# Kernel tuning notes

Hardware: AMD Instinct MI355X
Metric: run time of the kernel (lower is better)

Reference implementation:

```python
import jax, jax.numpy as jnp
import numpy as np

HIDDEN = 1024
NUM_HEADS = 16
BATCH = 2
SEQ = 2048


def setup_inputs() -> dict:
    key = jax.random.key(0)
    ks = jax.random.split(key, 5)
    scale = 1.0 / np.sqrt(HIDDEN)
    return {
        "x": jax.random.normal(ks[0], (BATCH, SEQ, HIDDEN), dtype=jnp.float32),
        "W_qkv": jax.random.normal(ks[1], (HIDDEN, 3 * HIDDEN), dtype=jnp.float32) * scale,
        "b_qkv": jax.random.normal(ks[2], (3 * HIDDEN,), dtype=jnp.float32) * 0.02,
        "W_o": jax.random.normal(ks[3], (HIDDEN, HIDDEN), dtype=jnp.float32) * scale,
        "b_o": jax.random.normal(ks[4], (HIDDEN,), dtype=jnp.float32) * 0.02,
    }


def reference(x, W_qkv, b_qkv, W_o, b_o):
    # x: [B, S, H]
    B, S, H = x.shape
    nh = NUM_HEADS
    hs = H // nh
    qkv = jnp.einsum('bsh,hk->bsk', x, W_qkv) + b_qkv  # [B, S, 3H]
    Q, K, V = qkv[..., :H], qkv[..., H:2 * H], qkv[..., 2 * H:]
    # split heads: [B, nh, S, hs]
    Q = Q.reshape(B, S, nh, hs).transpose(0, 2, 1, 3)
    K = K.reshape(B, S, nh, hs).transpose(0, 2, 1, 3)
    V = V.reshape(B, S, nh, hs).transpose(0, 2, 1, 3)
    scores = jnp.einsum('bnqd,bnkd->bnqk', Q, K) / jnp.sqrt(jnp.asarray(hs, x.dtype))
    # NOTE: the original module applies no causal mask despite its name.
    probs = jax.nn.softmax(scores, axis=-1)
    av = jnp.einsum('bnqk,bnkd->bqnd', probs, V)  # [B, S, nh, hs]
    av = av.reshape(B, S, H)
    return jnp.einsum('bsh,ho->bso', av, W_o) + b_o
```

## Files before the change

### kernel.cpp

```cpp
#include <hip/hip_runtime.h>
#include <hip/hip_bf16.h>
#include <stdint.h>

#define HIDDEN 1024
#define NHEAD  16
#define HS     64
#define BATCH  2
#define SEQ    2048
#define MTOT   (BATCH*SEQ)
#define NQKV   (3*HIDDEN)

typedef __hip_bfloat16 bf16;
typedef __attribute__((ext_vector_type(8))) short s16x8;
typedef __attribute__((ext_vector_type(4))) float f32x4;
typedef __attribute__((ext_vector_type(16))) float f32x16;

__device__ __forceinline__ short f2bf(float f) {
  bf16 h = __float2bfloat16(f);
  return *reinterpret_cast<short*>(&h);
}

__device__ __forceinline__ unsigned cvt_pk_bf16(float lo, float hi) {
  unsigned r;
  asm("v_cvt_pk_bf16_f32 %0, %1, %2" : "=v"(r) : "v"(lo), "v"(hi));
  return r;
}

__device__ __forceinline__ int swz(int row, int blk) {
  return (row*8 + (blk ^ (row & 7)))*8;
}

#define GLOAD_LDS(gp, lp) \
  __builtin_amdgcn_global_load_lds((const __attribute__((address_space(1))) void*)(gp), \
                                   (__attribute__((address_space(3))) void*)(lp), 16, 0, 0)

__device__ __forceinline__ int xcd_swz(int orig, int nwg) {
  return (orig & 7)*(nwg >> 3) + (orig >> 3);
}

__global__ void k_cvt_x(const float* __restrict__ x, short* __restrict__ xb, int n8) {
  int i = blockIdx.x*256 + threadIdx.x;
  if (i >= n8) return;
  const f32x4* xv = (const f32x4*)x;
  f32x4 a = xv[2*i], b = xv[2*i+1];
  s16x8 o = { f2bf(a[0]), f2bf(a[1]), f2bf(a[2]), f2bf(a[3]),
              f2bf(b[0]), f2bf(b[1]), f2bf(b[2]), f2bf(b[3]) };
  *(s16x8*)&xb[i*8] = o;
}

__global__ void k_cvt_wT(const float* __restrict__ W, bf16* __restrict__ WT, int K, int N) {
  __shared__ __align__(16) float tile[64][65];
  int n0 = blockIdx.x*64, k0 = blockIdx.y*64;
  int t = threadIdx.x;
  #pragma unroll
  for (int c = 0; c < 4; c++) {
    int s = c*256 + t;
    int r = s >> 4;
    int cc = s & 15;
    f32x4 v = *(const f32x4*)&W[(size_t)(k0 + r)*N + n0 + cc*4];
    tile[r][cc*4+0] = v[0]; tile[r][cc*4+1] = v[1];
    tile[r][cc*4+2] = v[2]; tile[r][cc*4+3] = v[3];
  }
  __syncthreads();
  #pragma unroll
  for (int c = 0; c < 2; c++) {
    int s = c*256 + t;
    int r = s >> 3;
    int cc = s & 7;
    s16x8 o;
    #pragma unroll
    for (int u = 0; u < 8; u++) o[u] = f2bf(tile[cc*8+u][r]);
    *(s16x8*)&WT[(size_t)(n0 + r)*K + k0 + cc*8] = o;
  }
}

template<int OUT_BF16>
__global__ __launch_bounds__(256) void k_gemm(
    const bf16* __restrict__ A, const bf16* __restrict__ BT,
    const float* __restrict__ bias, void* __restrict__ Cout,
    int M, int N, int K)
{
  __shared__ __align__(16) short Asl[128*64];
  __shared__ __align__(16) short Bsl[128*64];
  int t = threadIdx.x;
  int lane = t & 63, w = t >> 6;
  int q = lane & 15, g = lane >> 4;
  int nwg = gridDim.x*gridDim.y;
  int swzid = xcd_swz(blockIdx.y*gridDim.x + blockIdx.x, nwg);
  int bx = swzid % gridDim.x, by = swzid / gridDim.x;
  int row0 = by*128, col0 = bx*128;
  int wr = (w >> 1)*64, wc = (w & 1)*64;

  f32x4 acc[4][4] = {};

  for (int kt = 0; kt < K; kt += 64) {
    __syncthreads();
    #pragma unroll
    for (int c = 0; c < 4; c++) {
      int s = c*256 + t, r = s >> 3, bd = s & 7, bs = bd ^ (r & 7);
      GLOAD_LDS(&A[(size_t)(row0 + r)*K + kt + bs*8], &Asl[s*8]);
      GLOAD_LDS(&BT[(size_t)(col0 + r)*K + kt + bs*8], &Bsl[s*8]);
    }
    __syncthreads();
    #pragma unroll
    for (int kk = 0; kk < 2; kk++) {
      s16x8 af[4], bfr[4];
      #pragma unroll
      for (int i = 0; i < 4; i++) {
        af[i]  = *(const s16x8*)&Asl[swz(wr + i*16 + q, kk*4 + g)];
        bfr[i] = *(const s16x8*)&Bsl[swz(wc + i*16 + q, kk*4 + g)];
      }
      __builtin_amdgcn_s_setprio(1);
      #pragma unroll
      for (int i = 0; i < 4; i++)
        #pragma unroll
        for (int j = 0; j < 4; j++)
          acc[i][j] = __builtin_amdgcn_mfma_f32_16x16x32_bf16(af[i], bfr[j], acc[i][j], 0, 0, 0);
      __builtin_amdgcn_s_setprio(0);
    }
  }
  #pragma unroll
  for (int i = 0; i < 4; i++) {
    #pragma unroll
    for (int j = 0; j < 4; j++) {
      int col = col0 + wc + j*16 + q;
      float bv = bias[col];
      int rowb = row0 + wr + i*16 + g*4;
      #pragma unroll
      for (int r = 0; r < 4; r++) {
        float v = acc[i][j][r] + bv;
        if (OUT_BF16)
          ((bf16*)Cout)[(size_t)(rowb + r)*N + col] = __float2bfloat16(v);
        else
          ((float*)Cout)[(size_t)(rowb + r)*N + col] = v;
      }
    }
  }
}

__global__ void k_repack_v(const bf16* __restrict__ qkv, bf16* __restrict__ Vt) {
  int s0 = blockIdx.x*64;
  int bh = blockIdx.y;
  int b = bh >> 4, h = bh & 15;
  __shared__ __align__(16) short vt[64][68];
  int t = threadIdx.x;
  #pragma unroll
  for (int c = 0; c < 2; c++) {
    int s = c*256 + t, r = s >> 3, bd = s & 7;
    s16x8 v = *(const s16x8*)&qkv[(size_t)(b*SEQ + s0 + r)*NQKV + 2*HIDDEN + h*HS + bd*8];
    #pragma unroll
    for (int u = 0; u < 8; u++) vt[r][bd*8+u] = v[u];
  }
  __syncthreads();
  #pragma unroll
  for (int c = 0; c < 2; c++) {
    int s = c*256 + t, d = s >> 3, bs8 = s & 7;
    s16x8 o;
    #pragma unroll
    for (int u = 0; u < 8; u++) {
      int p = bs8*8 + u;
      int key = (p & ~12) | ((p & 4) << 1) | ((p & 8) >> 1);
      o[u] = vt[key][d];
    }
    *(s16x8*)&Vt[((size_t)(bh*HS + d))*SEQ + s0 + bs8*8] = o;
  }
}

struct AttnState {
  float psum;
  f32x16 oacc0, oacc1;
};

__device__ __forceinline__ void attn_stage(
    const bf16* __restrict__ kbase, const bf16* __restrict__ vbase,
    int kv, int t, short* Ks, short* Vs)
{
  #pragma unroll
  for (int c = 0; c < 4; c++) {
    int s = c*256 + t, r = s >> 3, bd = s & 7, bs = bd ^ (r & 7);
    GLOAD_LDS(&kbase[(size_t)(kv + r)*NQKV + bs*8], &Ks[s*8]);
  }
  #pragma unroll
  for (int c = 0; c < 4; c++) {
    int s = c*256 + t, d = s >> 4, bd = s & 15, bs = bd ^ (d & 15);
    GLOAD_LDS(&vbase[(size_t)d*SEQ + kv + bs*8], &Vs[s*8]);
  }
}

__device__ __forceinline__ void attn_compute(
    const short* Ks, const short* Vs, const s16x8* qf,
    int ql, int hi, AttnState& st)
{
  const float SC2 = 0.125f*1.44269504f;
  const float CB  = -12.f*1.44269504f;
  #pragma unroll
  for (int kb = 0; kb < 4; kb++) {
    f32x16 sf = {};
    __builtin_amdgcn_s_setprio(1);
    #pragma unroll
    for (int ks = 0; ks < 4; ks++) {
      int row = kb*32 + ql;
      int ch = (ks*2 + hi) ^ (row & 7);
      s16x8 a = *(const s16x8*)&Ks[(row*8 + ch)*8];
      sf = __builtin_amdgcn_mfma_f32_32x32x16_bf16(a, qf[ks], sf, 0, 0, 0);
    }
    __builtin_amdgcn_s_setprio(0);

    unsigned pkw[8];
    #pragma unroll
    for (int i = 0; i < 8; i++) {
      float p0 = __builtin_amdgcn_exp2f(__builtin_fmaf(sf[2*i],   SC2, CB));
      float p1 = __builtin_amdgcn_exp2f(__builtin_fmaf(sf[2*i+1], SC2, CB));
      st.psum += p0 + p1;
      pkw[i] = cvt_pk_bf16(p0, p1);
    }

    __builtin_amdgcn_s_setprio(1);
    #pragma unroll
    for (int kq = 0; kq < 2; kq++) {
      union { unsigned u[4]; s16x8 v; } pu;
      pu.u[0] = pkw[kq*4]; pu.u[1] = pkw[kq*4+1];
      pu.u[2] = pkw[kq*4+2]; pu.u[3] = pkw[kq*4+3];
      s16x8 pa = pu.v;
      {
        int row = ql, ch = (kb*4 + kq*2 + hi) ^ (row & 15);
        s16x8 vb = *(const s16x8*)&Vs[(row*16 + ch)*8];
        st.oacc0 = __builtin_amdgcn_mfma_f32_32x32x16_bf16(pa, vb, st.oacc0, 0, 0, 0);
      }
      {
        int row = 32 + ql, ch = (kb*4 + kq*2 + hi) ^ (row & 15);
        s16x8 vb = *(const s16x8*)&Vs[(row*16 + ch)*8];
        st.oacc1 = __builtin_amdgcn_mfma_f32_32x32x16_bf16(pa, vb, st.oacc1, 0, 0, 0);
      }
    }
    __builtin_amdgcn_s_setprio(0);
  }
}

__global__ __launch_bounds__(256) void k_attn(
    const bf16* __restrict__ qkv, const bf16* __restrict__ Vt, bf16* __restrict__ av)
{
  __shared__ __align__(16) short Ks0[128*64], Ks1[128*64];
  __shared__ __align__(16) short Vs0[64*128], Vs1[64*128];
  int t = threadIdx.x;
  int lane = t & 63, w = t >> 6;
  int ql = lane & 31, hi = lane >> 5;
  int nwg = gridDim.x*gridDim.y;
  int swzid = xcd_swz(blockIdx.y*gridDim.x + blockIdx.x, nwg);
  int qt = swzid & 15, bh = swzid >> 4;
  int b = bh >> 4, h = bh & 15;

  const bf16* qrow = qkv + (size_t)(b*SEQ + qt*128 + w*32 + ql)*NQKV + h*HS;
  s16x8 qf[4];
  #pragma unroll
  for (int ks = 0; ks < 4; ks++)
    qf[ks] = *(const s16x8*)&qrow[ks*16 + hi*8];

  AttnState st;
  st.psum = 0.f;
  st.oacc0 = (f32x16){}; st.oacc1 = (f32x16){};

  const bf16* kbase = qkv + (size_t)(b*SEQ)*NQKV + HIDDEN + h*HS;
  const bf16* vbase = Vt + (size_t)(bh*HS)*SEQ;

  attn_stage(kbase, vbase, 0, t, Ks0, Vs0);
  __syncthreads();

  #pragma unroll 1
  for (int tt = 0; tt < SEQ/128; tt += 2) {
    int kv = tt*128;
    if (kv + 128 < SEQ) attn_stage(kbase, vbase, kv + 128, t, Ks1, Vs1);
    attn_compute(Ks0, Vs0, qf, ql, hi, st);
    __syncthreads();
    if (kv + 256 < SEQ) attn_stage(kbase, vbase, kv + 256, t, Ks0, Vs0);
    attn_compute(Ks1, Vs1, qf, ql, hi, st);
    __syncthreads();
  }

  float psum = st.psum + __shfl_xor(st.psum, 32);
  float linv = 1.f/psum;

  #pragma unroll
  for (int r = 0; r < 16; r++) {
    int qr = (r & 3) + 8*(r >> 2) + 4*hi;
    float lr = __shfl(linv, qr);
    int row = b*SEQ + qt*128 + w*32 + qr;
    bf16* orow = av + (size_t)row*HIDDEN + h*HS;
    orow[ql]      = __float2bfloat16(st.oacc0[r]*lr);
    orow[32 + ql] = __float2bfloat16(st.oacc1[r]*lr);
  }
}

extern "C" void kernel_launch(void* const* d_in, const int* in_sizes, int n_in,
                              void* d_out, int out_size, void* d_ws, size_t ws_size,
                              hipStream_t stream) {
  const float* x    = (const float*)d_in[0];
  const float* Wqkv = (const float*)d_in[1];
  const float* bqkv = (const float*)d_in[2];
  const float* Wo   = (const float*)d_in[3];
  const float* bo   = (const float*)d_in[4];

  char* ws = (char*)d_ws;
  bf16* xb    = (bf16*)(ws);
  bf16* av    = xb;
  bf16* WqkvT = (bf16*)(ws + (8  << 20));
  bf16* WoT   = (bf16*)(ws + (14 << 20));
  bf16* qkv   = (bf16*)(ws + (16 << 20));
  bf16* Vt    = (bf16*)(ws + (40 << 20));

  k_cvt_x<<<dim3(MTOT*HIDDEN/8/256), 256, 0, stream>>>(x, (short*)xb, MTOT*HIDDEN/8);
  k_cvt_wT<<<dim3(NQKV/64, HIDDEN/64), 256, 0, stream>>>(Wqkv, WqkvT, HIDDEN, NQKV);
  k_cvt_wT<<<dim3(HIDDEN/64, HIDDEN/64), 256, 0, stream>>>(Wo, WoT, HIDDEN, HIDDEN);
  k_gemm<1><<<dim3(NQKV/128, MTOT/128), 256, 0, stream>>>(xb, WqkvT, bqkv, qkv, MTOT, NQKV, HIDDEN);
  k_repack_v<<<dim3(SEQ/64, BATCH*NHEAD), 256, 0, stream>>>(qkv, Vt);
  k_attn<<<dim3(SEQ/128, BATCH*NHEAD), 256, 0, stream>>>(qkv, Vt, av);
  k_gemm<0><<<dim3(HIDDEN/128, MTOT/128), 256, 0, stream>>>(av, WoT, bo, d_out, MTOT, HIDDEN, HIDDEN);
}
```

Before: 118.6 us.

## Process 64 query rows per wave in attention to reuse K/V LDS fragments

Each wave now handles two 32-row query blocks instead of one. K and V fragments are loaded from LDS once and reused for both blocks, and the workgroup covers 256 queries, so the grid is halved. This cuts LDS reads and global K/V staging per query. The cost is twice the accumulator registers, fewer workgroups (256 instead of 512), and a launch_bounds occupancy hint that could cause register spills.

```diff
diff --git a/kernel.cpp b/kernel.cpp
--- a/kernel.cpp
+++ b/kernel.cpp
@@ -166,11 +166,6 @@
   }
 }
 
-struct AttnState {
-  float psum;
-  f32x16 oacc0, oacc1;
-};
-
 __device__ __forceinline__ void attn_stage(
     const bf16* __restrict__ kbase, const bf16* __restrict__ vbase,
     int kv, int t, short* Ks, short* Vs)
@@ -187,57 +182,71 @@
   }
 }
 
+struct AttnState {
+  float psum[2];
+  f32x16 oacc[2][2];
+};
+
 __device__ __forceinline__ void attn_compute(
-    const short* Ks, const short* Vs, const s16x8* qf,
+    const short* Ks, const short* Vs, const s16x8 qf[2][4],
     int ql, int hi, AttnState& st)
 {
   const float SC2 = 0.125f*1.44269504f;
   const float CB  = -12.f*1.44269504f;
   #pragma unroll
   for (int kb = 0; kb < 4; kb++) {
-    f32x16 sf = {};
-    __builtin_amdgcn_s_setprio(1);
+    s16x8 ka[4];
+    int krow = kb*32 + ql;
     #pragma unroll
     for (int ks = 0; ks < 4; ks++) {
-      int row = kb*32 + ql;
-      int ch = (ks*2 + hi) ^ (row & 7);
-      s16x8 a = *(const s16x8*)&Ks[(row*8 + ch)*8];
-      sf = __builtin_amdgcn_mfma_f32_32x32x16_bf16(a, qf[ks], sf, 0, 0, 0);
-    }
-    __builtin_amdgcn_s_setprio(0);
-
-    unsigned pkw[8];
-    #pragma unroll
-    for (int i = 0; i < 8; i++) {
-      float p0 = __builtin_amdgcn_exp2f(__builtin_fmaf(sf[2*i],   SC2, CB));
-      float p1 = __builtin_amdgcn_exp2f(__builtin_fmaf(sf[2*i+1], SC2, CB));
-      st.psum += p0 + p1;
-      pkw[i] = cvt_pk_bf16(p0, p1);
-    }
-
-    __builtin_amdgcn_s_setprio(1);
+      int ch = (ks*2 + hi) ^ (krow & 7);
+      ka[ks] = *(const s16x8*)&Ks[(krow*8 + ch)*8];
+    }
+    s16x8 vfrag[2][2];
     #pragma unroll
     for (int kq = 0; kq < 2; kq++) {
-      union { unsigned u[4]; s16x8 v; } pu;
-      pu.u[0] = pkw[kq*4]; pu.u[1] = pkw[kq*4+1];
-      pu.u[2] = pkw[kq*4+2]; pu.u[3] = pkw[kq*4+3];
-      s16x8 pa = pu.v;
-      {
-        int row = ql, ch = (kb*4 + kq*2 + hi) ^ (row & 15);
-        s16x8 vb = *(const s16x8*)&Vs[(row*16 + ch)*8];
-        st.oacc0 = __builtin_amdgcn_mfma_f32_32x32x16_bf16(pa, vb, st.oacc0, 0, 0, 0);
-      }
-      {
-        int row = 32 + ql, ch = (kb*4 + kq*2 + hi) ^ (row & 15);
-        s16x8 vb = *(const s16x8*)&Vs[(row*16 + ch)*8];
-        st.oacc1 = __builtin_amdgcn_mfma_f32_32x32x16_bf16(pa, vb, st.oacc1, 0, 0, 0);
-      }
-    }
-    __builtin_amdgcn_s_setprio(0);
-  }
-}
-
-__global__ __launch_bounds__(256) void k_attn(
+      #pragma unroll
+      for (int db = 0; db < 2; db++) {
+        int row = db*32 + ql;
+        int ch = (kb*4 + kq*2 + hi) ^ (row & 15);
+        vfrag[kq][db] = *(const s16x8*)&Vs[(row*16 + ch)*8];
+      }
+    }
+    #pragma unroll
+    for (int qb = 0; qb < 2; qb++) {
+      f32x16 sf = {};
+      __builtin_amdgcn_s_setprio(1);
+      #pragma unroll
+      for (int ks = 0; ks < 4; ks++)
+        sf = __builtin_amdgcn_mfma_f32_32x32x16_bf16(ka[ks], qf[qb][ks], sf, 0, 0, 0);
+      __builtin_amdgcn_s_setprio(0);
+
+      unsigned pkw[8];
+      #pragma unroll
+      for (int i = 0; i < 8; i++) {
+        float p0 = __builtin_amdgcn_exp2f(__builtin_fmaf(sf[2*i],   SC2, CB));
+        float p1 = __builtin_amdgcn_exp2f(__builtin_fmaf(sf[2*i+1], SC2, CB));
+        st.psum[qb] += p0 + p1;
+        pkw[i] = cvt_pk_bf16(p0, p1);
+      }
+
+      __builtin_amdgcn_s_setprio(1);
+      #pragma unroll
+      for (int kq = 0; kq < 2; kq++) {
+        union { unsigned u[4]; s16x8 v; } pu;
+        pu.u[0] = pkw[kq*4]; pu.u[1] = pkw[kq*4+1];
+        pu.u[2] = pkw[kq*4+2]; pu.u[3] = pkw[kq*4+3];
+        s16x8 pa = pu.v;
+        #pragma unroll
+        for (int db = 0; db < 2; db++)
+          st.oacc[qb][db] = __builtin_amdgcn_mfma_f32_32x32x16_bf16(pa, vfrag[kq][db], st.oacc[qb][db], 0, 0, 0);
+      }
+      __builtin_amdgcn_s_setprio(0);
+    }
+  }
+}
+
+__global__ __launch_bounds__(256, 2) void k_attn(
     const bf16* __restrict__ qkv, const bf16* __restrict__ Vt, bf16* __restrict__ av)
 {
   __shared__ __align__(16) short Ks0[128*64], Ks1[128*64];
@@ -247,18 +256,22 @@
   int ql = lane & 31, hi = lane >> 5;
   int nwg = gridDim.x*gridDim.y;
   int swzid = xcd_swz(blockIdx.y*gridDim.x + blockIdx.x, nwg);
-  int qt = swzid & 15, bh = swzid >> 4;
+  int qt = swzid & 7, bh = swzid >> 3;
   int b = bh >> 4, h = bh & 15;
 
-  const bf16* qrow = qkv + (size_t)(b*SEQ + qt*128 + w*32 + ql)*NQKV + h*HS;
-  s16x8 qf[4];
-  #pragma unroll
-  for (int ks = 0; ks < 4; ks++)
-    qf[ks] = *(const s16x8*)&qrow[ks*16 + hi*8];
+  s16x8 qf[2][4];
+  #pragma unroll
+  for (int qb = 0; qb < 2; qb++) {
+    const bf16* qrow = qkv + (size_t)(b*SEQ + qt*256 + w*64 + qb*32 + ql)*NQKV + h*HS;
+    #pragma unroll
+    for (int ks = 0; ks < 4; ks++)
+      qf[qb][ks] = *(const s16x8*)&qrow[ks*16 + hi*8];
+  }
 
   AttnState st;
-  st.psum = 0.f;
-  st.oacc0 = (f32x16){}; st.oacc1 = (f32x16){};
+  st.psum[0] = 0.f; st.psum[1] = 0.f;
+  st.oacc[0][0] = (f32x16){}; st.oacc[0][1] = (f32x16){};
+  st.oacc[1][0] = (f32x16){}; st.oacc[1][1] = (f32x16){};
 
   const bf16* kbase = qkv + (size_t)(b*SEQ)*NQKV + HIDDEN + h*HS;
   const bf16* vbase = Vt + (size_t)(bh*HS)*SEQ;
@@ -277,17 +290,24 @@
     __syncthreads();
   }
 
-  float psum = st.psum + __shfl_xor(st.psum, 32);
-  float linv = 1.f/psum;
-
-  #pragma unroll
-  for (int r = 0; r < 16; r++) {
-    int qr = (r & 3) + 8*(r >> 2) + 4*hi;
-    float lr = __shfl(linv, qr);
-    int row = b*SEQ + qt*128 + w*32 + qr;
-    bf16* orow = av + (size_t)row*HIDDEN + h*HS;
-    orow[ql]      = __float2bfloat16(st.oacc0[r]*lr);
-    orow[32 + ql] = __float2bfloat16(st.oacc1[r]*lr);
+  float linv[2];
+  #pragma unroll
+  for (int qb = 0; qb < 2; qb++) {
+    float ps = st.psum[qb] + __shfl_xor(st.psum[qb], 32);
+    linv[qb] = 1.f/ps;
+  }
+
+  #pragma unroll
+  for (int qb = 0; qb < 2; qb++) {
+    #pragma unroll
+    for (int r = 0; r < 16; r++) {
+      int qr = (r & 3) + 8*(r >> 2) + 4*hi;
+      float lr = __shfl(linv[qb], qr);
+      int row = b*SEQ + qt*256 + w*64 + qb*32 + qr;
+      bf16* orow = av + (size_t)row*HIDDEN + h*HS;
+      orow[ql]      = __float2bfloat16(st.oacc[qb][0][r]*lr);
+      orow[32 + ql] = __float2bfloat16(st.oacc[qb][1][r]*lr);
+    }
   }
 }
 
@@ -313,6 +333,6 @@
   k_cvt_wT<<<dim3(HIDDEN/64, HIDDEN/64), 256, 0, stream>>>(Wo, WoT, HIDDEN, HIDDEN);
   k_gemm<1><<<dim3(NQKV/128, MTOT/128), 256, 0, stream>>>(xb, WqkvT, bqkv, qkv, MTOT, NQKV, HIDDEN);
   k_repack_v<<<dim3(SEQ/64, BATCH*NHEAD), 256, 0, stream>>>(qkv, Vt);
-  k_attn<<<dim3(SEQ/128, BATCH*NHEAD), 256, 0, stream>>>(qkv, Vt, av);
+  k_attn<<<dim3(SEQ/256, BATCH*NHEAD), 256, 0, stream>>>(qkv, Vt, av);
   k_gemm<0><<<dim3(HIDDEN/128, MTOT/128), 256, 0, stream>>>(av, WoT, bo, d_out, MTOT, HIDDEN, HIDDEN);
 }
```

Result: slower. 167.9 us (+41.5%).
